# Kernel optimization log

Measured on AMD Instinct MI355X. Metric: run time of the kernel, lower is better.

The kernel has to match this reference:

```python
import jax, jax.numpy as jnp
import numpy as np

N_NODES = 50000
N_EDGES = 1200000
IN_SIZE = 128
HID = 64
OUT = 64
NEG_SLOPE = 0.01  # torch F.leaky_relu default


def setup_inputs() -> dict:
    key = jax.random.key(0)
    ks = jax.random.split(key, 8)
    x = jax.random.normal(ks[0], (N_NODES, IN_SIZE), dtype=jnp.float32)
    edge_weight = jax.random.uniform(ks[1], (N_EDGES,), dtype=jnp.float32)
    W1 = jax.random.normal(ks[2], (IN_SIZE, HID), dtype=jnp.float32) / np.sqrt(IN_SIZE)
    b1 = jax.random.normal(ks[3], (HID,), dtype=jnp.float32) * 0.01
    W2 = jax.random.normal(ks[4], (HID, OUT), dtype=jnp.float32) / np.sqrt(HID)
    b2 = jax.random.normal(ks[5], (OUT,), dtype=jnp.float32) * 0.01
    src = jax.random.randint(ks[6], (N_EDGES,), 0, N_NODES, dtype=jnp.int64 if jax.config.jax_enable_x64 else jnp.int32)
    dst = jax.random.randint(ks[7], (N_EDGES,), 0, N_NODES, dtype=jnp.int64 if jax.config.jax_enable_x64 else jnp.int32)
    return {"x": x, "edge_weight": edge_weight, "W1": W1, "b1": b1,
            "W2": W2, "b2": b2, "src": src, "dst": dst}


def _wg_layer(h, W, b, src, dst, edge_weight, n_nodes):
    # Linear projection on all nodes: [N, d_out]
    Wh = h @ W + b
    # u_mul_e: gather source features, scale by scalar edge weight -> [E, d_out]
    msg = Wh[src] * edge_weight[:, None]
    # fn.mean('m','h'): segment-mean by destination node
    s = jax.ops.segment_sum(msg, dst, num_segments=n_nodes)
    deg = jax.ops.segment_sum(jnp.ones_like(edge_weight), dst, num_segments=n_nodes)
    return s / jnp.maximum(deg, 1.0)[:, None]  # isolated nodes -> 0 (DGL default)


def reference(x, edge_weight, W1, b1, W2, b2, src, dst):
    n = x.shape[0]
    h1 = _wg_layer(x, W1, b1, src, dst, edge_weight, n)
    h1 = jax.nn.leaky_relu(h1, negative_slope=NEG_SLOPE)
    out = _wg_layer(h1, W2, b2, src, dst, edge_weight, n)
    return out
```

## Files before the change

### kernel.cpp

```cpp
#include <hip/hip_runtime.h>
#include <hip/hip_fp16.h>


#define N_NODES 50000
#define N_EDGES 1200000
#define IN_SIZE 128
#define HID 64
#define NEG_SLOPE 0.01f
#define NBB 391
#define SLOTC 3456
#define FILL_EPB 8192
#define FILL_BLOCKS ((N_EDGES + FILL_EPB - 1) / FILL_EPB)
#define GEMM_BLOCKS ((N_NODES + 255) / 256)
#define RS2 (HID + 8)

typedef _Float16 half8 __attribute__((ext_vector_type(8)));
typedef float floatx4 __attribute__((ext_vector_type(4)));

template <int K>
__device__ __forceinline__ void gemm_body(int blk,
                                          const float* __restrict__ A,
                                          const float* __restrict__ W,
                                          const float* __restrict__ b,
                                          _Float16* __restrict__ out,
                                          _Float16* wthi, _Float16* wtlo) {
    constexpr int RS = K + 8;
    const int tid = threadIdx.x;
    for (int i = tid; i < 64 * K; i += 1024) {
        int n = i / K, k = i % K;
        float wv = W[k * 64 + n];
        _Float16 hi = (_Float16)wv;
        wthi[n * RS + k] = hi;
        wtlo[n * RS + k] = (_Float16)(wv - (float)hi);
    }
    __syncthreads();

    const int lane = tid & 63;
    const int wid = tid >> 6;
    const int q = lane >> 4, c = lane & 15;

    int arow = blk * 256 + wid * 16 + c;
    int lrow = min(arow, N_NODES - 1);
    const float* ap = A + (size_t)lrow * K + q * 8;

    floatx4 acc0 = {b[c],      b[c],      b[c],      b[c]};
    floatx4 acc1 = {b[c + 16], b[c + 16], b[c + 16], b[c + 16]};
    floatx4 acc2 = {b[c + 32], b[c + 32], b[c + 32], b[c + 32]};
    floatx4 acc3 = {b[c + 48], b[c + 48], b[c + 48], b[c + 48]};

#pragma unroll
    for (int ks = 0; ks < K / 32; ++ks) {
        float4 f0 = ((const float4*)(ap + ks * 32))[0];
        float4 f1 = ((const float4*)(ap + ks * 32))[1];
        float fv[8] = {f0.x, f0.y, f0.z, f0.w, f1.x, f1.y, f1.z, f1.w};
        half8 ahi, alo;
#pragma unroll
        for (int j = 0; j < 8; ++j) {
            _Float16 h = (_Float16)fv[j];
            ahi[j] = h;
            alo[j] = (_Float16)(fv[j] - (float)h);
        }
        const int kb = ks * 32 + q * 8;
        half8 bh0 = *(const half8*)&wthi[(c     ) * RS + kb];
        half8 bl0 = *(const half8*)&wtlo[(c     ) * RS + kb];
        half8 bh1 = *(const half8*)&wthi[(c + 16) * RS + kb];
        half8 bl1 = *(const half8*)&wtlo[(c + 16) * RS + kb];
        half8 bh2 = *(const half8*)&wthi[(c + 32) * RS + kb];
        half8 bl2 = *(const half8*)&wtlo[(c + 32) * RS + kb];
        half8 bh3 = *(const half8*)&wthi[(c + 48) * RS + kb];
        half8 bl3 = *(const half8*)&wtlo[(c + 48) * RS + kb];
        acc0 = __builtin_amdgcn_mfma_f32_16x16x32_f16(ahi, bh0, acc0, 0, 0, 0);
        acc0 = __builtin_amdgcn_mfma_f32_16x16x32_f16(ahi, bl0, acc0, 0, 0, 0);
        acc0 = __builtin_amdgcn_mfma_f32_16x16x32_f16(alo, bh0, acc0, 0, 0, 0);
        acc1 = __builtin_amdgcn_mfma_f32_16x16x32_f16(ahi, bh1, acc1, 0, 0, 0);
        acc1 = __builtin_amdgcn_mfma_f32_16x16x32_f16(ahi, bl1, acc1, 0, 0, 0);
        acc1 = __builtin_amdgcn_mfma_f32_16x16x32_f16(alo, bh1, acc1, 0, 0, 0);
        acc2 = __builtin_amdgcn_mfma_f32_16x16x32_f16(ahi, bh2, acc2, 0, 0, 0);
        acc2 = __builtin_amdgcn_mfma_f32_16x16x32_f16(ahi, bl2, acc2, 0, 0, 0);
        acc2 = __builtin_amdgcn_mfma_f32_16x16x32_f16(alo, bh2, acc2, 0, 0, 0);
        acc3 = __builtin_amdgcn_mfma_f32_16x16x32_f16(ahi, bh3, acc3, 0, 0, 0);
        acc3 = __builtin_amdgcn_mfma_f32_16x16x32_f16(ahi, bl3, acc3, 0, 0, 0);
        acc3 = __builtin_amdgcn_mfma_f32_16x16x32_f16(alo, bh3, acc3, 0, 0, 0);
    }

    int rowb = blk * 256 + wid * 16 + q * 4;
#pragma unroll
    for (int r = 0; r < 4; ++r) {
        if (rowb + r < N_NODES) {
            _Float16* op = out + (size_t)(rowb + r) * HID + c;
            op[0]  = (_Float16)acc0[r];
            op[16] = (_Float16)acc1[r];
            op[32] = (_Float16)acc2[r];
            op[48] = (_Float16)acc3[r];
        }
    }
}

struct FillLds {
    unsigned int spay[FILL_EPB];
    unsigned short saux[FILL_EPB];
    int lhist[NBB];
    int lbase[NBB];
    int lstart[NBB];
    int wsum[8];
};

__device__ __forceinline__ void fill_body(int blk,
                                          const int* __restrict__ src,
                                          const int* __restrict__ dst,
                                          const float* __restrict__ ew,
                                          int* __restrict__ gcur,
                                          unsigned int* __restrict__ epay,
                                          unsigned char* __restrict__ ed7,
                                          FillLds& f) {
    const int tid = threadIdx.x;
    const int e0 = blk * FILL_EPB;
    const int nblk = min(FILL_EPB, N_EDGES - e0);
    if (tid < NBB) f.lhist[tid] = 0;

    const int g0 = e0 + 4 * tid, g1 = g0 + 4096;
    const bool a0 = g0 < N_EDGES, a1 = g1 < N_EDGES;
    int4 d0 = {0,0,0,0}, d1 = {0,0,0,0}, s0 = {0,0,0,0}, s1 = {0,0,0,0};
    float4 w0 = {0,0,0,0}, w1 = {0,0,0,0};
    if (a0) { d0 = *(const int4*)(dst + g0); s0 = *(const int4*)(src + g0);
              w0 = *(const float4*)(ew + g0); }
    if (a1) { d1 = *(const int4*)(dst + g1); s1 = *(const int4*)(src + g1);
              w1 = *(const float4*)(ew + g1); }
    __syncthreads();

    if (a0) { atomicAdd(&f.lhist[d0.x >> 7], 1); atomicAdd(&f.lhist[d0.y >> 7], 1);
              atomicAdd(&f.lhist[d0.z >> 7], 1); atomicAdd(&f.lhist[d0.w >> 7], 1); }
    if (a1) { atomicAdd(&f.lhist[d1.x >> 7], 1); atomicAdd(&f.lhist[d1.y >> 7], 1);
              atomicAdd(&f.lhist[d1.z >> 7], 1); atomicAdd(&f.lhist[d1.w >> 7], 1); }
    __syncthreads();

    int orig = 0, v = 0;
    if (tid < NBB) {
        orig = f.lhist[tid];
        v = orig;
        for (int o = 1; o < 64; o <<= 1) {
            int t = __shfl_up(v, o);
            if ((tid & 63) >= o) v += t;
        }
        if ((tid & 63) == 63 || tid == NBB - 1) f.wsum[tid >> 6] = v;
    }
    __syncthreads();
    if (tid < NBB) {
        int w = tid >> 6;
        int incl = v;
        for (int k = 0; k < w; ++k) incl += f.wsum[k];
        int excl = incl - orig;
        f.lstart[tid] = excl;
        int gb = orig ? atomicAdd(&gcur[tid], orig) : 0;
        f.lbase[tid] = tid * SLOTC + gb - excl;
        f.lhist[tid] = 0;
    }
    __syncthreads();

    const int dd0[4] = {d0.x, d0.y, d0.z, d0.w};
    const int ss0[4] = {s0.x, s0.y, s0.z, s0.w};
    const float ww0[4] = {w0.x, w0.y, w0.z, w0.w};
    const int dd1[4] = {d1.x, d1.y, d1.z, d1.w};
    const int ss1[4] = {s1.x, s1.y, s1.z, s1.w};
    const float ww1[4] = {w1.x, w1.y, w1.z, w1.w};
    if (a0) {
#pragma unroll
        for (int j = 0; j < 4; ++j) {
            int d = dd0[j], b = d >> 7;
            unsigned short hw = __half_as_ushort(__float2half(ww0[j]));
            int pos = f.lstart[b] + atomicAdd(&f.lhist[b], 1);
            f.spay[pos] = (unsigned int)(ss0[j] & 0xffff) | ((unsigned int)hw << 16);
            f.saux[pos] = (unsigned short)((d & 127) | (b << 7));
        }
    }
    if (a1) {
#pragma unroll
        for (int j = 0; j < 4; ++j) {
            int d = dd1[j], b = d >> 7;
            unsigned short hw = __half_as_ushort(__float2half(ww1[j]));
            int pos = f.lstart[b] + atomicAdd(&f.lhist[b], 1);
            f.spay[pos] = (unsigned int)(ss1[j] & 0xffff) | ((unsigned int)hw << 16);
            f.saux[pos] = (unsigned short)((d & 127) | (b << 7));
        }
    }
    __syncthreads();

    for (int i = tid; i < nblk; i += 1024) {
        int aux = f.saux[i];
        int b = aux >> 7;
        int gi = f.lbase[b] + i;
        if (gi < (b + 1) * SLOTC) {
            epay[gi] = f.spay[i];
            ed7[gi] = (unsigned char)(aux & 127);
        }
    }
}

__global__ __launch_bounds__(1024) void fill_gemm1(const int* __restrict__ src,
                                                   const int* __restrict__ dst,
                                                   const float* __restrict__ ew,
                                                   int* __restrict__ gcur,
                                                   unsigned int* __restrict__ epay,
                                                   unsigned char* __restrict__ ed7,
                                                   const float* __restrict__ x,
                                                   const float* __restrict__ W1,
                                                   const float* __restrict__ b1,
                                                   _Float16* __restrict__ outA) {
    __shared__ union SU {
        FillLds f;
        struct { _Float16 hi[64 * (IN_SIZE + 8)];
                 _Float16 lo[64 * (IN_SIZE + 8)]; } g;
    } u;
    if (blockIdx.x < FILL_BLOCKS)
        fill_body(blockIdx.x, src, dst, ew, gcur, epay, ed7, u.f);
    else
        gemm_body<IN_SIZE>(blockIdx.x - FILL_BLOCKS, x, W1, b1, outA,
                           u.g.hi, u.g.lo);
}

__global__ __launch_bounds__(1024) void sort_agg1_gemm2(
        const int* __restrict__ gcur,
        const unsigned int* __restrict__ epay,
        const unsigned char* __restrict__ ed7,
        const _Float16* __restrict__ Wh1,
        const float* __restrict__ W2, const float* __restrict__ b2,
        unsigned int* __restrict__ esort, int* __restrict__ off,
        _Float16* __restrict__ outB) {
    __shared__ unsigned int lsort[SLOTC];
    __shared__ int cnt[128];
    __shared__ int start[128];
    __shared__ int wsum[2];
    __shared__ _Float16 w2hi[64 * RS2];
    __shared__ _Float16 w2lo[64 * RS2];
    __shared__ union AU {
        struct { unsigned int pay[SLOTC]; unsigned char d7[SLOTC]; } s;
        _Float16 hs[128 * RS2];
    } u;
    const int tid = threadIdx.x;
    const int bkt = blockIdx.x;
    const int beg = bkt * SLOTC;
    const int n = min(gcur[bkt], SLOTC);

    for (int i = tid; i < 64 * HID; i += 1024) {
        int nn = i >> 6, k = i & 63;
        float wv = W2[k * 64 + nn];
        _Float16 hi = (_Float16)wv;
        w2hi[nn * RS2 + k] = hi;
        w2lo[nn * RS2 + k] = (_Float16)(wv - (float)hi);
    }
    if (tid < 128) cnt[tid] = 0;
    __syncthreads();

    for (int e = tid; e < n; e += 1024) {
        int d7 = ed7[beg + e];
        u.s.pay[e] = epay[beg + e];
        u.s.d7[e] = (unsigned char)d7;
        atomicAdd(&cnt[d7], 1);
    }
    __syncthreads();

    int orig = 0, incl = 0;
    if (tid < 128) {
        orig = cnt[tid];
        int v = orig;
        for (int o = 1; o < 64; o <<= 1) {
            int t = __shfl_up(v, o);
            if ((tid & 63) >= o) v += t;
        }
        if ((tid & 63) == 63) wsum[tid >> 6] = v;
        incl = v;
    }
    __syncthreads();
    if (tid < 128) {
        if (tid >= 64) incl += wsum[0];
        int excl = incl - orig;
        start[tid] = excl;
        off[bkt * 129 + tid] = beg + excl;
        if (tid == 127) off[bkt * 129 + 128] = beg + incl;
        cnt[tid] = 0;
    }
    __syncthreads();

    for (int e = tid; e < n; e += 1024) {
        int d7 = u.s.d7[e];
        int pos = atomicAdd(&cnt[d7], 1);
        int idx = start[d7] + pos;
        if (idx < SLOTC)
            lsort[idx] = u.s.pay[e];
    }
    __syncthreads();

    for (int i = tid; i < n; i += 1024)
        esort[beg + i] = lsort[i];

    {
        const int lane = tid & 63;
        const int g = lane >> 3, p = lane & 7;
        const int nl = (tid >> 6) * 8 + g;
        const int lbeg = start[nl];
        const int deg = cnt[nl];
        float acc[8] = {0, 0, 0, 0, 0, 0, 0, 0};
        const int lend = min(lbeg + deg, SLOTC);
        for (int e = lbeg; e < lend; ++e) {
            const unsigned int pe = lsort[e];
            const float w =
                __half2float(__ushort_as_half((unsigned short)(pe >> 16)));
            half8 row = *(const half8*)(Wh1 + (size_t)(pe & 0xffff) * HID + p * 8);
#pragma unroll
            for (int j = 0; j < 8; ++j)
                acc[j] = fmaf((float)row[j], w, acc[j]);
        }
        const float inv = 1.0f / fmaxf((float)deg, 1.0f);
        half8 hv;
#pragma unroll
        for (int j = 0; j < 8; ++j) {
            float t = acc[j] * inv;
            t = t >= 0.0f ? t : NEG_SLOPE * t;
            hv[j] = (_Float16)t;
        }
        *(half8*)&u.hs[nl * RS2 + p * 8] = hv;
    }
    __syncthreads();

    {
        const int lane = tid & 63, wid = tid >> 6;
        const int q = lane >> 4, c = lane & 15;
        const int r = wid >> 1, ch = wid & 1;
        floatx4 acc0 = {b2[ch * 32 + c], b2[ch * 32 + c],
                        b2[ch * 32 + c], b2[ch * 32 + c]};
        floatx4 acc1 = {b2[ch * 32 + 16 + c], b2[ch * 32 + 16 + c],
                        b2[ch * 32 + 16 + c], b2[ch * 32 + 16 + c]};
#pragma unroll
        for (int ks = 0; ks < 2; ++ks) {
            const int kb = ks * 32 + q * 8;
            half8 a = *(const half8*)&u.hs[(r * 16 + c) * RS2 + kb];
            half8 bh0 = *(const half8*)&w2hi[(ch * 32 + c) * RS2 + kb];
            half8 bl0 = *(const half8*)&w2lo[(ch * 32 + c) * RS2 + kb];
            half8 bh1 = *(const half8*)&w2hi[(ch * 32 + 16 + c) * RS2 + kb];
            half8 bl1 = *(const half8*)&w2lo[(ch * 32 + 16 + c) * RS2 + kb];
            acc0 = __builtin_amdgcn_mfma_f32_16x16x32_f16(a, bh0, acc0, 0, 0, 0);
            acc0 = __builtin_amdgcn_mfma_f32_16x16x32_f16(a, bl0, acc0, 0, 0, 0);
            acc1 = __builtin_amdgcn_mfma_f32_16x16x32_f16(a, bh1, acc1, 0, 0, 0);
            acc1 = __builtin_amdgcn_mfma_f32_16x16x32_f16(a, bl1, acc1, 0, 0, 0);
        }
        const int rowb = bkt * 128 + r * 16 + q * 4;
#pragma unroll
        for (int rr = 0; rr < 4; ++rr) {
            if (rowb + rr < N_NODES) {
                _Float16* op = outB + (size_t)(rowb + rr) * HID + ch * 32 + c;
                op[0]  = (_Float16)acc0[rr];
                op[16] = (_Float16)acc1[rr];
            }
        }
    }
}

__global__ __launch_bounds__(256) void agg2_k(const _Float16* __restrict__ Wh,
                                              const int* __restrict__ off,
                                              const unsigned int* __restrict__ es,
                                              float* __restrict__ out) {
    const int tid = threadIdx.x;
    const int lane = tid & 63;
    const int wid = tid >> 6;
    const int g = lane >> 3, p = lane & 7;
    const int node = blockIdx.x * 32 + wid * 8 + g;
    const bool valid = node < N_NODES;
    int beg = 0, end = 0;
    if (valid) {
        const int o = (node >> 7) * 129 + (node & 127);
        beg = off[o];
        end = off[o + 1];
    }
    const int deg = end - beg;

    unsigned int pld[5];
#pragma unroll
    for (int c = 0; c < 5; ++c) {
        int e = beg + c * 8 + p;
        pld[c] = (e < end) ? es[e] : 0u;
    }

    int mdeg = deg;
#pragma unroll
    for (int mask = 8; mask <= 32; mask <<= 1)
        mdeg = max(mdeg, __shfl_xor(mdeg, mask));

    float acc[8] = {0, 0, 0, 0, 0, 0, 0, 0};
#pragma unroll
    for (int c = 0; c < 5; ++c) {
        if (c * 8 >= mdeg) break;
#pragma unroll
        for (int s = 0; s < 8; ++s) {
            const unsigned int pe = __shfl(pld[c], (g << 3) | s);
            const bool act = beg + c * 8 + s < end;
            const int srow = act ? (int)(pe & 0xffff) : 0;
            const float w = act
                ? __half2float(__ushort_as_half((unsigned short)(pe >> 16)))
                : 0.0f;
            half8 row = *(const half8*)(Wh + (size_t)srow * HID + p * 8);
#pragma unroll
            for (int j = 0; j < 8; ++j)
                acc[j] = fmaf((float)row[j], w, acc[j]);
        }
    }
    for (int e = beg + 40; e < end; ++e) {
        const unsigned int pe = es[e];
        const float w =
            __half2float(__ushort_as_half((unsigned short)(pe >> 16)));
        half8 row = *(const half8*)(Wh + (size_t)(pe & 0xffff) * HID + p * 8);
#pragma unroll
        for (int j = 0; j < 8; ++j)
            acc[j] = fmaf((float)row[j], w, acc[j]);
    }

    if (valid) {
        const float inv = 1.0f / fmaxf((float)deg, 1.0f);
        float4* op = (float4*)(out + (size_t)node * HID + p * 8);
        op[0] = make_float4(acc[0] * inv, acc[1] * inv, acc[2] * inv, acc[3] * inv);
        op[1] = make_float4(acc[4] * inv, acc[5] * inv, acc[6] * inv, acc[7] * inv);
    }
}

extern "C" void kernel_launch(void* const* d_in, const int* in_sizes, int n_in,
                              void* d_out, int out_size, void* d_ws, size_t ws_size,
                              hipStream_t stream) {
    const float* x  = (const float*)d_in[0];
    const float* ew = (const float*)d_in[1];
    const float* W1 = (const float*)d_in[2];
    const float* b1 = (const float*)d_in[3];
    const float* W2 = (const float*)d_in[4];
    const float* b2 = (const float*)d_in[5];
    const int* src  = (const int*)d_in[6];
    const int* dst  = (const int*)d_in[7];
    float* out = (float*)d_out;

    const int NH = N_NODES * HID;
    const int ES = NBB * SLOTC;

    int* gcur = (int*)d_ws;
    int* off  = gcur + 400;
    unsigned int* esort = (unsigned int*)(off + 50448);
    unsigned int* epay = esort + ES;
    unsigned char* ed7 = (unsigned char*)(epay + ES);
    _Float16* bufA = (_Float16*)(ed7 + ES);
    _Float16* bufB = bufA + NH;

    const int agg2Blocks = (N_NODES + 31) / 32;

    hipMemsetAsync(gcur, 0, 400 * sizeof(int), stream);

    fill_gemm1<<<FILL_BLOCKS + GEMM_BLOCKS, 1024, 0, stream>>>(
        src, dst, ew, gcur, epay, ed7, x, W1, b1, bufA);

    sort_agg1_gemm2<<<NBB, 1024, 0, stream>>>(
        gcur, epay, ed7, bufA, W2, b2, esort, off, bufB);

    agg2_k<<<agg2Blocks, 256, 0, stream>>>(bufB, off, esort, out);
}
```

Before: 74.30 us.

## Halve bucket size to 64 nodes and use 512-thread sort blocks

```diff
diff --git a/kernel.cpp b/kernel.cpp
--- a/kernel.cpp
+++ b/kernel.cpp
@@ -7,8 +7,8 @@
 #define IN_SIZE 128
 #define HID 64
 #define NEG_SLOPE 0.01f
-#define NBB 391
-#define SLOTC 3456
+#define NBB 782
+#define SLOTC 1856
 #define FILL_EPB 8192
 #define FILL_BLOCKS ((N_EDGES + FILL_EPB - 1) / FILL_EPB)
 #define GEMM_BLOCKS ((N_NODES + 255) / 256)
@@ -102,7 +102,7 @@
     int lhist[NBB];
     int lbase[NBB];
     int lstart[NBB];
-    int wsum[8];
+    int wsum[16];
 };
 
 __device__ __forceinline__ void fill_body(int blk,
@@ -111,7 +111,7 @@
                                           const float* __restrict__ ew,
                                           int* __restrict__ gcur,
                                           unsigned int* __restrict__ epay,
-                                          unsigned char* __restrict__ ed7,
+                                          unsigned char* __restrict__ ed6,
                                           FillLds& f) {
     const int tid = threadIdx.x;
     const int e0 = blk * FILL_EPB;
@@ -128,10 +128,10 @@
               w1 = *(const float4*)(ew + g1); }
     __syncthreads();
 
-    if (a0) { atomicAdd(&f.lhist[d0.x >> 7], 1); atomicAdd(&f.lhist[d0.y >> 7], 1);
-              atomicAdd(&f.lhist[d0.z >> 7], 1); atomicAdd(&f.lhist[d0.w >> 7], 1); }
-    if (a1) { atomicAdd(&f.lhist[d1.x >> 7], 1); atomicAdd(&f.lhist[d1.y >> 7], 1);
-              atomicAdd(&f.lhist[d1.z >> 7], 1); atomicAdd(&f.lhist[d1.w >> 7], 1); }
+    if (a0) { atomicAdd(&f.lhist[d0.x >> 6], 1); atomicAdd(&f.lhist[d0.y >> 6], 1);
+              atomicAdd(&f.lhist[d0.z >> 6], 1); atomicAdd(&f.lhist[d0.w >> 6], 1); }
+    if (a1) { atomicAdd(&f.lhist[d1.x >> 6], 1); atomicAdd(&f.lhist[d1.y >> 6], 1);
+              atomicAdd(&f.lhist[d1.z >> 6], 1); atomicAdd(&f.lhist[d1.w >> 6], 1); }
     __syncthreads();
 
     int orig = 0, v = 0;
@@ -166,32 +166,32 @@
     if (a0) {
 #pragma unroll
         for (int j = 0; j < 4; ++j) {
-            int d = dd0[j], b = d >> 7;
+            int d = dd0[j], b = d >> 6;
             unsigned short hw = __half_as_ushort(__float2half(ww0[j]));
             int pos = f.lstart[b] + atomicAdd(&f.lhist[b], 1);
             f.spay[pos] = (unsigned int)(ss0[j] & 0xffff) | ((unsigned int)hw << 16);
-            f.saux[pos] = (unsigned short)((d & 127) | (b << 7));
+            f.saux[pos] = (unsigned short)((d & 63) | (b << 6));
         }
     }
     if (a1) {
 #pragma unroll
         for (int j = 0; j < 4; ++j) {
-            int d = dd1[j], b = d >> 7;
+            int d = dd1[j], b = d >> 6;
             unsigned short hw = __half_as_ushort(__float2half(ww1[j]));
             int pos = f.lstart[b] + atomicAdd(&f.lhist[b], 1);
             f.spay[pos] = (unsigned int)(ss1[j] & 0xffff) | ((unsigned int)hw << 16);
-            f.saux[pos] = (unsigned short)((d & 127) | (b << 7));
+            f.saux[pos] = (unsigned short)((d & 63) | (b << 6));
         }
     }
     __syncthreads();
 
     for (int i = tid; i < nblk; i += 1024) {
         int aux = f.saux[i];
-        int b = aux >> 7;
+        int b = aux >> 6;
         int gi = f.lbase[b] + i;
         if (gi < (b + 1) * SLOTC) {
             epay[gi] = f.spay[i];
-            ed7[gi] = (unsigned char)(aux & 127);
+            ed6[gi] = (unsigned char)(aux & 63);
         }
     }
 }
@@ -201,7 +201,7 @@
                                                    const float* __restrict__ ew,
                                                    int* __restrict__ gcur,
                                                    unsigned int* __restrict__ epay,
-                                                   unsigned char* __restrict__ ed7,
+                                                   unsigned char* __restrict__ ed6,
                                                    const float* __restrict__ x,
                                                    const float* __restrict__ W1,
                                                    const float* __restrict__ b1,
@@ -212,91 +212,92 @@
                  _Float16 lo[64 * (IN_SIZE + 8)]; } g;
     } u;
     if (blockIdx.x < FILL_BLOCKS)
-        fill_body(blockIdx.x, src, dst, ew, gcur, epay, ed7, u.f);
+        fill_body(blockIdx.x, src, dst, ew, gcur, epay, ed6, u.f);
     else
         gemm_body<IN_SIZE>(blockIdx.x - FILL_BLOCKS, x, W1, b1, outA,
                            u.g.hi, u.g.lo);
 }
 
-__global__ __launch_bounds__(1024) void sort_agg1_gemm2(
+__global__ __launch_bounds__(512, 8) void sort_agg1_gemm2(
         const int* __restrict__ gcur,
         const unsigned int* __restrict__ epay,
-        const unsigned char* __restrict__ ed7,
+        const unsigned char* __restrict__ ed6,
         const _Float16* __restrict__ Wh1,
         const float* __restrict__ W2, const float* __restrict__ b2,
         unsigned int* __restrict__ esort, int* __restrict__ off,
         _Float16* __restrict__ outB) {
     __shared__ unsigned int lsort[SLOTC];
-    __shared__ int cnt[128];
-    __shared__ int start[128];
-    __shared__ int wsum[2];
+    __shared__ int cnt[64];
+    __shared__ int start[64];
     __shared__ _Float16 w2hi[64 * RS2];
     __shared__ _Float16 w2lo[64 * RS2];
-    __shared__ union AU {
-        struct { unsigned int pay[SLOTC]; unsigned char d7[SLOTC]; } s;
-        _Float16 hs[128 * RS2];
-    } u;
+    __shared__ _Float16 hs[64 * RS2];
     const int tid = threadIdx.x;
     const int bkt = blockIdx.x;
     const int beg = bkt * SLOTC;
     const int n = min(gcur[bkt], SLOTC);
 
-    for (int i = tid; i < 64 * HID; i += 1024) {
+    for (int i = tid; i < 64 * HID; i += 512) {
         int nn = i >> 6, k = i & 63;
         float wv = W2[k * 64 + nn];
         _Float16 hi = (_Float16)wv;
         w2hi[nn * RS2 + k] = hi;
         w2lo[nn * RS2 + k] = (_Float16)(wv - (float)hi);
     }
-    if (tid < 128) cnt[tid] = 0;
-    __syncthreads();
-
-    for (int e = tid; e < n; e += 1024) {
-        int d7 = ed7[beg + e];
-        u.s.pay[e] = epay[beg + e];
-        u.s.d7[e] = (unsigned char)d7;
-        atomicAdd(&cnt[d7], 1);
-    }
-    __syncthreads();
-
-    int orig = 0, incl = 0;
-    if (tid < 128) {
-        orig = cnt[tid];
+    if (tid < 64) cnt[tid] = 0;
+    __syncthreads();
+
+    const int e4 = 4 * tid;
+    uint4 p4 = {0, 0, 0, 0};
+    unsigned int dv = 0;
+    int m = 0;
+    if (e4 < n) {
+        p4 = *(const uint4*)(epay + beg + e4);
+        dv = *(const unsigned int*)(ed6 + beg + e4);
+        m = min(4, n - e4);
+        const unsigned int pp[4] = {p4.x, p4.y, p4.z, p4.w};
+#pragma unroll
+        for (int j = 0; j < 4; ++j)
+            if (j < m) atomicAdd(&cnt[(dv >> (8 * j)) & 63], 1);
+        (void)pp;
+    }
+    __syncthreads();
+
+    if (tid < 64) {
+        int orig = cnt[tid];
         int v = orig;
         for (int o = 1; o < 64; o <<= 1) {
             int t = __shfl_up(v, o);
-            if ((tid & 63) >= o) v += t;
-        }
-        if ((tid & 63) == 63) wsum[tid >> 6] = v;
-        incl = v;
-    }
-    __syncthreads();
-    if (tid < 128) {
-        if (tid >= 64) incl += wsum[0];
-        int excl = incl - orig;
-        start[tid] = excl;
-        off[bkt * 129 + tid] = beg + excl;
-        if (tid == 127) off[bkt * 129 + 128] = beg + incl;
+            if (tid >= o) v += t;
+        }
+        start[tid] = v - orig;
+        off[bkt * 65 + tid] = beg + v - orig;
+        if (tid == 63) off[bkt * 65 + 64] = beg + v;
         cnt[tid] = 0;
     }
     __syncthreads();
 
-    for (int e = tid; e < n; e += 1024) {
-        int d7 = u.s.d7[e];
-        int pos = atomicAdd(&cnt[d7], 1);
-        int idx = start[d7] + pos;
-        if (idx < SLOTC)
-            lsort[idx] = u.s.pay[e];
-    }
-    __syncthreads();
-
-    for (int i = tid; i < n; i += 1024)
-        esort[beg + i] = lsort[i];
-
+    if (m) {
+        const unsigned int pp[4] = {p4.x, p4.y, p4.z, p4.w};
+#pragma unroll
+        for (int j = 0; j < 4; ++j) {
+            if (j < m) {
+                int d6 = (dv >> (8 * j)) & 63;
+                int pos = atomicAdd(&cnt[d6], 1);
+                int idx = start[d6] + pos;
+                if (idx < SLOTC) {
+                    lsort[idx] = pp[j];
+                    esort[beg + idx] = pp[j];
+                }
+            }
+        }
+    }
+    __syncthreads();
+
+    const int lane = tid & 63;
+    const int g = lane >> 3, p = lane & 7;
+    const int nl = (tid >> 6) * 8 + g;
     {
-        const int lane = tid & 63;
-        const int g = lane >> 3, p = lane & 7;
-        const int nl = (tid >> 6) * 8 + g;
         const int lbeg = start[nl];
         const int deg = cnt[nl];
         float acc[8] = {0, 0, 0, 0, 0, 0, 0, 0};
@@ -318,12 +319,12 @@
             t = t >= 0.0f ? t : NEG_SLOPE * t;
             hv[j] = (_Float16)t;
         }
-        *(half8*)&u.hs[nl * RS2 + p * 8] = hv;
+        *(half8*)&hs[nl * RS2 + p * 8] = hv;
     }
     __syncthreads();
 
     {
-        const int lane = tid & 63, wid = tid >> 6;
+        const int wid = tid >> 6;
         const int q = lane >> 4, c = lane & 15;
         const int r = wid >> 1, ch = wid & 1;
         floatx4 acc0 = {b2[ch * 32 + c], b2[ch * 32 + c],
@@ -333,7 +334,7 @@
 #pragma unroll
         for (int ks = 0; ks < 2; ++ks) {
             const int kb = ks * 32 + q * 8;
-            half8 a = *(const half8*)&u.hs[(r * 16 + c) * RS2 + kb];
+            half8 a = *(const half8*)&hs[(r * 16 + c) * RS2 + kb];
             half8 bh0 = *(const half8*)&w2hi[(ch * 32 + c) * RS2 + kb];
             half8 bl0 = *(const half8*)&w2lo[(ch * 32 + c) * RS2 + kb];
             half8 bh1 = *(const half8*)&w2hi[(ch * 32 + 16 + c) * RS2 + kb];
@@ -343,7 +344,7 @@
             acc1 = __builtin_amdgcn_mfma_f32_16x16x32_f16(a, bh1, acc1, 0, 0, 0);
             acc1 = __builtin_amdgcn_mfma_f32_16x16x32_f16(a, bl1, acc1, 0, 0, 0);
         }
-        const int rowb = bkt * 128 + r * 16 + q * 4;
+        const int rowb = bkt * 64 + r * 16 + q * 4;
 #pragma unroll
         for (int rr = 0; rr < 4; ++rr) {
             if (rowb + rr < N_NODES) {
@@ -367,7 +368,7 @@
     const bool valid = node < N_NODES;
     int beg = 0, end = 0;
     if (valid) {
-        const int o = (node >> 7) * 129 + (node & 127);
+        const int o = (node >> 6) * 65 + (node & 63);
         beg = off[o];
         end = off[o + 1];
     }
@@ -438,22 +439,22 @@
     const int ES = NBB * SLOTC;
 
     int* gcur = (int*)d_ws;
-    int* off  = gcur + 400;
-    unsigned int* esort = (unsigned int*)(off + 50448);
+    int* off  = gcur + 784;
+    unsigned int* esort = (unsigned int*)(off + 50832);
     unsigned int* epay = esort + ES;
-    unsigned char* ed7 = (unsigned char*)(epay + ES);
-    _Float16* bufA = (_Float16*)(ed7 + ES);
+    unsigned char* ed6 = (unsigned char*)(epay + ES);
+    _Float16* bufA = (_Float16*)(ed6 + ES);
     _Float16* bufB = bufA + NH;
 
     const int agg2Blocks = (N_NODES + 31) / 32;
 
-    hipMemsetAsync(gcur, 0, 400 * sizeof(int), stream);
+    hipMemsetAsync(gcur, 0, 784 * sizeof(int), stream);
 
     fill_gemm1<<<FILL_BLOCKS + GEMM_BLOCKS, 1024, 0, stream>>>(
-        src, dst, ew, gcur, epay, ed7, x, W1, b1, bufA);
-
-    sort_agg1_gemm2<<<NBB, 1024, 0, stream>>>(
-        gcur, epay, ed7, bufA, W2, b2, esort, off, bufB);
+        src, dst, ew, gcur, epay, ed6, x, W1, b1, bufA);
+
+    sort_agg1_gemm2<<<NBB, 512, 0, stream>>>(
+        gcur, epay, ed6, bufA, W2, b2, esort, off, bufB);
 
     agg2_k<<<agg2Blocks, 256, 0, stream>>>(bufB, off, esort, out);
 }
```

New measurement: 78.82 us. 6.1% more time.
